# Kernel optimization log

Measured on AMD Instinct MI355X. Metric: run time of the kernel, lower is better.

The kernel has to match this reference:

```python
import jax, jax.numpy as jnp
import numpy as np

N_QUBITS = 10
T_STEPS = 10
NDATA = 1024
DIM = 2 ** N_QUBITS
PI = float(np.pi)


def setup_inputs() -> dict:
    key = jax.random.key(0)
    k1, k2, k3, k4, k5 = jax.random.split(key, 5)
    # random complex amplitudes (normalized to unit states inside reference)
    inputs_re = jax.random.normal(k1, (NDATA, DIM), dtype=jnp.float32)
    inputs_im = jax.random.normal(k2, (NDATA, DIM), dtype=jnp.float32)
    # diffusion noise schedule diff_hs (t,) in (0,1]
    diff_hs = jax.random.uniform(k5, (T_STEPS,), dtype=jnp.float32, minval=0.1, maxval=1.0)
    # var_1 = diff_hs.repeat(3n) in torch == tile -> index k scaled by diff_hs[k % t]
    var_1 = jnp.tile(diff_hs, 3 * N_QUBITS)                                  # (3*n*t,)
    phis = (jax.random.uniform(k3, (NDATA, 3 * N_QUBITS * T_STEPS), dtype=jnp.float32)
            * (PI / 4.0) - (PI / 8.0)) * var_1[None, :]
    gs = (jax.random.uniform(k4, (NDATA, T_STEPS), dtype=jnp.float32) * 0.2 + 0.4) * diff_hs[None, :]
    return {"inputs_re": inputs_re, "inputs_im": inputs_im, "phis": phis, "gs": gs}


def _apply_1q(psi, M, i):
    """Apply per-sample 2x2 gate M (B,2,2) on qubit i (qubit 0 = MSB) to psi (B, 2**n)."""
    left = 2 ** i
    right = 2 ** (N_QUBITS - 1 - i)
    s = psi.reshape(NDATA, left, 2, right)
    s = jnp.einsum('bxy,bayc->baxc', M, s)
    return s.reshape(NDATA, DIM)


def _scramble(inputs_re, inputs_im, phis, gs):
    n, t = N_QUBITS, T_STEPS
    psi = (inputs_re + 1j * inputs_im).astype(jnp.complex64)
    psi = psi / jnp.linalg.norm(psi, axis=1, keepdims=True)  # unit input states

    # precompute sum_{i<j} z_i z_j per basis state for the diagonal RZZ product
    idx = jnp.arange(DIM)
    bits = (idx[:, None] >> jnp.arange(n - 1, -1, -1)[None, :]) & 1  # (DIM, n), qubit0=MSB
    z = 1.0 - 2.0 * bits.astype(jnp.float32)
    zsum = z.sum(axis=1)
    pairsum = 0.5 * (zsum ** 2 - n)                                   # (DIM,)
    inv = 1.0 / (2.0 * np.sqrt(float(n)))

    for tt in range(t):
        base = 3 * n * tt
        for i in range(n):
            a = phis[:, base + i]            # first RZ angle
            th = phis[:, base + n + i]       # RY angle
            b = phis[:, base + 2 * n + i]    # second RZ angle
            c = jnp.cos(0.5 * th).astype(jnp.complex64)
            s = jnp.sin(0.5 * th).astype(jnp.complex64)
            ea_m = jnp.exp(-0.5j * a); ea_p = jnp.exp(0.5j * a)
            eb_m = jnp.exp(-0.5j * b); eb_p = jnp.exp(0.5j * b)
            # M = RZ(b) @ RY(th) @ RZ(a), per sample (B,2,2)
            M = jnp.stack([
                jnp.stack([eb_m * c * ea_m, -eb_m * s * ea_p], axis=-1),
                jnp.stack([eb_p * s * ea_m,  eb_p * c * ea_p], axis=-1),
            ], axis=-2)
            psi = _apply_1q(psi, M, i)
        # all RZZ(i,j, theta) gates are diagonal with shared theta -> single fused phase
        theta = (gs[:, tt] * inv).astype(jnp.complex64)
        psi = psi * jnp.exp(-0.5j * theta[:, None] * pairsum[None, :])
    return psi


def reference(inputs_re, inputs_im, phis, gs):
    psi = _scramble(inputs_re, inputs_im, phis, gs)
    return jnp.stack([psi.real, psi.imag])  # (2, Ndata, 2**n) float32
```

## Files before the change

### kernel.cpp

```cpp
#include <hip/hip_runtime.h>

#define NQ 10
#define TS 10
#define DIM 1024
#define ND 1024

typedef _Float16 h4 __attribute__((ext_vector_type(4)));
typedef __fp16  p2 __attribute__((ext_vector_type(2)));
typedef float f4 __attribute__((ext_vector_type(4)));

__device__ __forceinline__ f4 mfma16(h4 a, h4 b, f4 c) {
    return __builtin_amdgcn_mfma_f32_16x16x16f16(a, b, c, 0, 0, 0);
}
__device__ __forceinline__ h4 cvt_h4(f4 x) {
    p2 lo = __builtin_amdgcn_cvt_pkrtz(x[0], x[1]);
    p2 hi = __builtin_amdgcn_cvt_pkrtz(x[2], x[3]);
    h4 r; r[0] = lo[0]; r[1] = lo[1]; r[2] = hi[0]; r[3] = hi[1];
    return r;
}
__device__ __forceinline__ float xsgn(float v, unsigned m) {
    return __uint_as_float(__float_as_uint(v) ^ m);
}

__global__ __launch_bounds__(64, 1) void qsim_kernel(
    const float* __restrict__ re_in, const float* __restrict__ im_in,
    const float* __restrict__ phis, const float* __restrict__ gs,
    float* __restrict__ out)
{
    const int sample = blockIdx.x;
    const int lane = threadIdx.x;
    const int quad = lane >> 4;
    const int cc = lane & 15;
    const int c3 = (cc >> 3) & 1, c2 = (cc >> 2) & 1, c1 = (cc >> 1) & 1, c0 = cc & 1;
    const int q1 = quad >> 1, q0 = quad & 1;

    const bool e31 = (c3 == q1);
    const bool e20 = (c2 == q0);
    const bool bc1 = (c1 != 0);
    const bool bc0 = (c0 != 0);
    const unsigned sg3 = c3 ? 0u : 0x80000000u;
    const unsigned sg2 = c2 ? 0u : 0x80000000u;

    const float* pr_in = re_in + sample * DIM;
    const float* pi_in = im_in + sample * DIM;
    const float* ph = phis + sample * (3 * NQ * TS);
    const float* gsp = gs + sample * TS;

    f4 Sr[4], Si[4];
    const int lbase = 256 * quad + cc;
#pragma unroll
    for (int n = 0; n < 4; ++n)
#pragma unroll
        for (int s = 0; s < 4; ++s) {
            Sr[n][s] = pr_in[lbase + 64 * s + 16 * n];
            Si[n][s] = pi_in[lbase + 64 * s + 16 * n];
        }

    const float inv = 0.15811388300841897f;
    float gk[TS];
#pragma unroll
    for (int t = 0; t < TS; ++t) gk[t] = -0.5f * (gsp[t] * inv);

    float nrm = 0.f;
#pragma unroll
    for (int n = 0; n < 4; ++n)
#pragma unroll
        for (int s = 0; s < 4; ++s) nrm += Sr[n][s] * Sr[n][s] + Si[n][s] * Si[n][s];
#pragma unroll
    for (int off = 32; off >= 1; off >>= 1) nrm += __shfl_xor(nrm, off, 64);
    const float scl = rsqrtf(nrm);
#pragma unroll
    for (int n = 0; n < 4; ++n) { Sr[n] *= scl; Si[n] *= scl; }

    float psv[4][4];
    const int pbase = __popc(quad) + __popc(cc);
#pragma unroll
    for (int n = 0; n < 4; ++n)
#pragma unroll
        for (int s = 0; s < 4; ++s) {
            const int p = pbase + __popc(n) + __popc(s);
            const int z = NQ - 2 * p;
            psv[n][s] = 0.5f * (float)(z * z - NQ);
        }
    const float fq1 = (float)q1, fq0 = (float)q0;
    const float fc3 = (float)c3, fc2 = (float)c2, fc1 = (float)c1, fc0 = (float)c0;

    f4 DCPv[4], DSPv[4];
    h4 gbb[2];
    h4 hbb[2][4][4];
    float bcur[NQ];

    auto make_trig = [&](const float* v, float kcur) {
        float sv = 0.f;
#pragma unroll
        for (int i = 0; i < NQ; ++i) sv += v[i];
        float base = -0.5f * sv;
        base = fmaf(fq1, v[0], base); base = fmaf(fq0, v[1], base);
        base = fmaf(fc3, v[6], base); base = fmaf(fc2, v[7], base);
        base = fmaf(fc1, v[8], base); base = fmaf(fc0, v[9], base);
        const float addS[4] = {0.f, v[3], v[2], v[2] + v[3]};
        const float addN[4] = {0.f, v[5], v[4], v[4] + v[5]};
#pragma unroll
        for (int n = 0; n < 4; ++n)
#pragma unroll
            for (int s = 0; s < 4; ++s) {
                const float phi = fmaf(kcur, psv[n][s], base + addN[n] + addS[s]);
                float sp, cp;
                __sincosf(phi, &sp, &cp);
                DCPv[n][s] = cp;
                DSPv[n][s] = sp;
            }
    };

    auto make_tiles = [&](const float* th, h4& gbo, h4 (&hbo)[4][4]) {
        float C[NQ], S[NQ];
#pragma unroll
        for (int g = 0; g < NQ; ++g) {
            float sg, cg;
            __sincosf(0.5f * th[g], &sg, &cg);
            S[g] = sg; C[g] = cg;
        }
        {
            const float g0 = e31 ? C[0] : xsgn(S[0], sg3);
            const float g1 = e20 ? C[1] : xsgn(S[1], sg2);
            const float f01 = g0 * g1;
            const float A0 = bc1 ? S[2] : C[2];
            const float A1 = bc1 ? C[2] : -S[2];
            const float B0 = bc0 ? S[3] : C[3];
            const float B1 = bc0 ? C[3] : -S[3];
            p2 lo = __builtin_amdgcn_cvt_pkrtz(f01 * A0 * B0, f01 * A0 * B1);
            p2 hi = __builtin_amdgcn_cvt_pkrtz(f01 * A1 * B0, f01 * A1 * B1);
            gbo[0] = lo[0]; gbo[1] = lo[1]; gbo[2] = hi[0]; gbo[3] = hi[1];
        }
        const float F67 = (e31 ? C[6] : xsgn(S[6], sg3)) * (e20 ? C[7] : xsgn(S[7], sg2));
        const float A0p = bc1 ? S[8] : C[8];
        const float A1p = bc1 ? C[8] : -S[8];
        const float B0p = bc0 ? S[9] : C[9];
        const float B1p = bc0 ? C[9] : -S[9];
        float W[4];
        W[0] = F67 * A0p * B0p; W[1] = F67 * A0p * B1p;
        W[2] = F67 * A1p * B0p; W[3] = F67 * A1p * B1p;
        const float P4[4] = {C[4] * C[5], C[4] * S[5], S[4] * C[5], S[4] * S[5]};
        float TP[4][4];
#pragma unroll
        for (int k = 0; k < 4; ++k)
#pragma unroll
            for (int s = 0; s < 4; ++s) TP[k][s] = P4[k] * W[s];
#pragma unroll
        for (int n = 0; n < 4; ++n)
#pragma unroll
            for (int j = 0; j < 4; ++j) {
                const int n1 = n >> 1, n0 = n & 1, j1 = j >> 1, j0 = j & 1;
                const int d1 = n1 ^ j1, d0 = n0 ^ j0;
                const int idx = d1 * 2 + d0;
                const float sg = (((d1 && !n1) ? -1.f : 1.f) * ((d0 && !n0) ? -1.f : 1.f));
                p2 lo = __builtin_amdgcn_cvt_pkrtz(sg * TP[idx][0], sg * TP[idx][1]);
                p2 hi = __builtin_amdgcn_cvt_pkrtz(sg * TP[idx][2], sg * TP[idx][3]);
                hbo[n][j][0] = lo[0]; hbo[n][j][1] = lo[1];
                hbo[n][j][2] = hi[0]; hbo[n][j][3] = hi[1];
            }
    };

    {
        float phs0[30];
#pragma unroll
        for (int j = 0; j < 30; ++j) phs0[j] = ph[j];
        make_trig(&phs0[0], 0.f);
        make_tiles(&phs0[10], gbb[0], hbb[0]);
#pragma unroll
        for (int i = 0; i < NQ; ++i) bcur[i] = phs0[20 + i];
    }
    float pipe[2][30];
#pragma unroll
    for (int j = 0; j < 30; ++j) pipe[0][j] = ph[30 + j];

    const f4 zf4 = {0.f, 0.f, 0.f, 0.f};

#pragma unroll
    for (int tt = 0; tt < TS; ++tt) {
#pragma unroll
        for (int n = 0; n < 4; ++n) {
            const f4 xr = Sr[n], xi = Si[n];
            Sr[n] = DCPv[n] * xr - DSPv[n] * xi;
            Si[n] = DSPv[n] * xr + DCPv[n] * xi;
        }

        if (tt + 2 < TS) {
#pragma unroll
            for (int j = 0; j < 30; ++j) pipe[(tt + 1) & 1][j] = ph[30 * (tt + 2) + j];
        }

        h4 ar[4], ai[4];
#pragma unroll
        for (int n = 0; n < 4; ++n) { ar[n] = cvt_h4(Sr[n]); ai[n] = cvt_h4(Si[n]); }
        f4 Tr[4], Ti[4];
#pragma unroll
        for (int n = 0; n < 4; ++n) {
            Tr[n] = mfma16(ar[n], gbb[tt & 1], zf4);
            Ti[n] = mfma16(ai[n], gbb[tt & 1], zf4);
        }

        if (tt + 1 < TS) {
            const float* pN = pipe[tt & 1];
            float vN[NQ];
#pragma unroll
            for (int i = 0; i < NQ; ++i) vN[i] = pN[i] + bcur[i];
            make_trig(vN, gk[tt]);
            make_tiles(&pN[10], gbb[(tt + 1) & 1], hbb[(tt + 1) & 1]);
#pragma unroll
            for (int i = 0; i < NQ; ++i) bcur[i] = pN[20 + i];
        } else {
            make_trig(bcur, gk[TS - 1]);
        }

        h4 tr[4], ti[4];
#pragma unroll
        for (int n = 0; n < 4; ++n) { tr[n] = cvt_h4(Tr[n]); ti[n] = cvt_h4(Ti[n]); }
#pragma unroll
        for (int n = 0; n < 4; ++n) {
            f4 r0 = mfma16(tr[0], hbb[tt & 1][n][0], zf4);
            r0 = mfma16(tr[1], hbb[tt & 1][n][1], r0);
            f4 r1 = mfma16(tr[2], hbb[tt & 1][n][2], zf4);
            r1 = mfma16(tr[3], hbb[tt & 1][n][3], r1);
            f4 i0 = mfma16(ti[0], hbb[tt & 1][n][0], zf4);
            i0 = mfma16(ti[1], hbb[tt & 1][n][1], i0);
            f4 i1 = mfma16(ti[2], hbb[tt & 1][n][2], zf4);
            i1 = mfma16(ti[3], hbb[tt & 1][n][3], i1);
            Sr[n] = r0 + r1;
            Si[n] = i0 + i1;
        }
    }

#pragma unroll
    for (int n = 0; n < 4; ++n) {
        const f4 xr = Sr[n], xi = Si[n];
        Sr[n] = DCPv[n] * xr - DSPv[n] * xi;
        Si[n] = DSPv[n] * xr + DCPv[n] * xi;
    }

    float* outr = out + sample * DIM;
    float* outi = out + ND * DIM + sample * DIM;
#pragma unroll
    for (int n = 0; n < 4; ++n)
#pragma unroll
        for (int s = 0; s < 4; ++s) {
            outr[lbase + 64 * s + 16 * n] = Sr[n][s];
            outi[lbase + 64 * s + 16 * n] = Si[n][s];
        }
}

extern "C" void kernel_launch(void* const* d_in, const int* in_sizes, int n_in,
                              void* d_out, int out_size, void* d_ws, size_t ws_size,
                              hipStream_t stream) {
    const float* re_in = (const float*)d_in[0];
    const float* im_in = (const float*)d_in[1];
    const float* phis  = (const float*)d_in[2];
    const float* gs    = (const float*)d_in[3];
    float* out = (float*)d_out;
    qsim_kernel<<<ND, 64, 0, stream>>>(re_in, im_in, phis, gs, out);
}
```

Measured before the change: 77.47 us.

## Split each sample's state across two wavefronts with LDS exchange per step

Each block now runs two wavefronts that each hold half of the 1024 amplitudes. The norm is reduced across waves through shared memory, and after the first MFMA stage each wave writes its partial tiles to LDS so both can read all four tiles for the second stage. This halves per-wave register state and trig/tile work, which should raise occupancy and parallelism. The cost is one barrier and an LDS round trip per time step. The register double-buffered prefetch of phis is replaced by a plain load at the start of each step.

```diff
diff --git a/kernel.cpp b/kernel.cpp
--- a/kernel.cpp
+++ b/kernel.cpp
@@ -22,13 +22,15 @@
     return __uint_as_float(__float_as_uint(v) ^ m);
 }
 
-__global__ __launch_bounds__(64, 1) void qsim_kernel(
+__global__ __launch_bounds__(128, 2) void qsim_kernel(
     const float* __restrict__ re_in, const float* __restrict__ im_in,
     const float* __restrict__ phis, const float* __restrict__ gs,
     float* __restrict__ out)
 {
     const int sample = blockIdx.x;
-    const int lane = threadIdx.x;
+    const int tid  = threadIdx.x;
+    const int wid  = tid >> 6;
+    const int lane = tid & 63;
     const int quad = lane >> 4;
     const int cc = lane & 15;
     const int c3 = (cc >> 3) & 1, c2 = (cc >> 2) & 1, c1 = (cc >> 1) & 1, c0 = cc & 1;
@@ -41,19 +43,23 @@
     const unsigned sg3 = c3 ? 0u : 0x80000000u;
     const unsigned sg2 = c2 ? 0u : 0x80000000u;
 
+    __shared__ h4 xch[2][4][2][64];
+    __shared__ float nsh[2];
+
     const float* pr_in = re_in + sample * DIM;
     const float* pi_in = im_in + sample * DIM;
     const float* ph = phis + sample * (3 * NQ * TS);
     const float* gsp = gs + sample * TS;
 
-    f4 Sr[4], Si[4];
+    f4 Sr[2], Si[2];
     const int lbase = 256 * quad + cc;
-#pragma unroll
-    for (int n = 0; n < 4; ++n)
+    const int noff = 32 * wid;
+#pragma unroll
+    for (int m = 0; m < 2; ++m)
 #pragma unroll
         for (int s = 0; s < 4; ++s) {
-            Sr[n][s] = pr_in[lbase + 64 * s + 16 * n];
-            Si[n][s] = pi_in[lbase + 64 * s + 16 * n];
+            Sr[m][s] = pr_in[lbase + 64 * s + noff + 16 * m];
+            Si[m][s] = pi_in[lbase + 64 * s + noff + 16 * m];
         }
 
     const float inv = 0.15811388300841897f;
@@ -63,31 +69,34 @@
 
     float nrm = 0.f;
 #pragma unroll
-    for (int n = 0; n < 4; ++n)
-#pragma unroll
-        for (int s = 0; s < 4; ++s) nrm += Sr[n][s] * Sr[n][s] + Si[n][s] * Si[n][s];
+    for (int m = 0; m < 2; ++m)
+#pragma unroll
+        for (int s = 0; s < 4; ++s) nrm += Sr[m][s] * Sr[m][s] + Si[m][s] * Si[m][s];
 #pragma unroll
     for (int off = 32; off >= 1; off >>= 1) nrm += __shfl_xor(nrm, off, 64);
-    const float scl = rsqrtf(nrm);
-#pragma unroll
-    for (int n = 0; n < 4; ++n) { Sr[n] *= scl; Si[n] *= scl; }
-
-    float psv[4][4];
-    const int pbase = __popc(quad) + __popc(cc);
-#pragma unroll
-    for (int n = 0; n < 4; ++n)
+    if (lane == 0) nsh[wid] = nrm;
+    __syncthreads();
+    const float scl = rsqrtf(nsh[0] + nsh[1]);
+#pragma unroll
+    for (int m = 0; m < 2; ++m) { Sr[m] *= scl; Si[m] *= scl; }
+
+    float psv[2][4];
+    const int pbase = __popc(quad) + __popc(cc) + wid;
+#pragma unroll
+    for (int m = 0; m < 2; ++m)
 #pragma unroll
         for (int s = 0; s < 4; ++s) {
-            const int p = pbase + __popc(n) + __popc(s);
+            const int p = pbase + m + __popc(s);
             const int z = NQ - 2 * p;
-            psv[n][s] = 0.5f * (float)(z * z - NQ);
+            psv[m][s] = 0.5f * (float)(z * z - NQ);
         }
     const float fq1 = (float)q1, fq0 = (float)q0;
     const float fc3 = (float)c3, fc2 = (float)c2, fc1 = (float)c1, fc0 = (float)c0;
-
-    f4 DCPv[4], DSPv[4];
+    const float fwid = (float)wid;
+
+    f4 DCPv[2], DSPv[2];
     h4 gbb[2];
-    h4 hbb[2][4][4];
+    h4 hbb[2][2][4];
     float bcur[NQ];
 
     auto make_trig = [&](const float* v, float kcur) {
@@ -98,21 +107,23 @@
         base = fmaf(fq1, v[0], base); base = fmaf(fq0, v[1], base);
         base = fmaf(fc3, v[6], base); base = fmaf(fc2, v[7], base);
         base = fmaf(fc1, v[8], base); base = fmaf(fc0, v[9], base);
+        base = fmaf(fwid, v[4], base);
         const float addS[4] = {0.f, v[3], v[2], v[2] + v[3]};
-        const float addN[4] = {0.f, v[5], v[4], v[4] + v[5]};
-#pragma unroll
-        for (int n = 0; n < 4; ++n)
+#pragma unroll
+        for (int m = 0; m < 2; ++m) {
+            const float bm = base + (m ? v[5] : 0.f);
 #pragma unroll
             for (int s = 0; s < 4; ++s) {
-                const float phi = fmaf(kcur, psv[n][s], base + addN[n] + addS[s]);
+                const float phi = fmaf(kcur, psv[m][s], bm + addS[s]);
                 float sp, cp;
                 __sincosf(phi, &sp, &cp);
-                DCPv[n][s] = cp;
-                DSPv[n][s] = sp;
+                DCPv[m][s] = cp;
+                DSPv[m][s] = sp;
             }
+        }
     };
 
-    auto make_tiles = [&](const float* th, h4& gbo, h4 (&hbo)[4][4]) {
+    auto make_tiles = [&](const float* th, h4& gbo, h4 (&hbo)[2][4]) {
         float C[NQ], S[NQ];
 #pragma unroll
         for (int g = 0; g < NQ; ++g) {
@@ -140,25 +151,21 @@
         float W[4];
         W[0] = F67 * A0p * B0p; W[1] = F67 * A0p * B1p;
         W[2] = F67 * A1p * B0p; W[3] = F67 * A1p * B1p;
-        const float P4[4] = {C[4] * C[5], C[4] * S[5], S[4] * C[5], S[4] * S[5]};
-        float TP[4][4];
-#pragma unroll
-        for (int k = 0; k < 4; ++k)
-#pragma unroll
-            for (int s = 0; s < 4; ++s) TP[k][s] = P4[k] * W[s];
-#pragma unroll
-        for (int n = 0; n < 4; ++n)
+        const float s4_0 = wid ? S[4] : C[4];
+        const float s4_1 = wid ? C[4] : -S[4];
+#pragma unroll
+        for (int m = 0; m < 2; ++m) {
+            const float s5_0 = m ? S[5] : C[5];
+            const float s5_1 = m ? C[5] : -S[5];
 #pragma unroll
             for (int j = 0; j < 4; ++j) {
-                const int n1 = n >> 1, n0 = n & 1, j1 = j >> 1, j0 = j & 1;
-                const int d1 = n1 ^ j1, d0 = n0 ^ j0;
-                const int idx = d1 * 2 + d0;
-                const float sg = (((d1 && !n1) ? -1.f : 1.f) * ((d0 && !n0) ? -1.f : 1.f));
-                p2 lo = __builtin_amdgcn_cvt_pkrtz(sg * TP[idx][0], sg * TP[idx][1]);
-                p2 hi = __builtin_amdgcn_cvt_pkrtz(sg * TP[idx][2], sg * TP[idx][3]);
-                hbo[n][j][0] = lo[0]; hbo[n][j][1] = lo[1];
-                hbo[n][j][2] = hi[0]; hbo[n][j][3] = hi[1];
+                const float v45 = ((j >> 1) ? s4_1 : s4_0) * ((j & 1) ? s5_1 : s5_0);
+                p2 lo = __builtin_amdgcn_cvt_pkrtz(v45 * W[0], v45 * W[1]);
+                p2 hi = __builtin_amdgcn_cvt_pkrtz(v45 * W[2], v45 * W[3]);
+                hbo[m][j][0] = lo[0]; hbo[m][j][1] = lo[1];
+                hbo[m][j][2] = hi[0]; hbo[m][j][3] = hi[1];
             }
+        }
     };
 
     {
@@ -170,82 +177,91 @@
 #pragma unroll
         for (int i = 0; i < NQ; ++i) bcur[i] = phs0[20 + i];
     }
-    float pipe[2][30];
-#pragma unroll
-    for (int j = 0; j < 30; ++j) pipe[0][j] = ph[30 + j];
 
     const f4 zf4 = {0.f, 0.f, 0.f, 0.f};
 
 #pragma unroll
     for (int tt = 0; tt < TS; ++tt) {
-#pragma unroll
-        for (int n = 0; n < 4; ++n) {
-            const f4 xr = Sr[n], xi = Si[n];
-            Sr[n] = DCPv[n] * xr - DSPv[n] * xi;
-            Si[n] = DSPv[n] * xr + DCPv[n] * xi;
-        }
-
-        if (tt + 2 < TS) {
-#pragma unroll
-            for (int j = 0; j < 30; ++j) pipe[(tt + 1) & 1][j] = ph[30 * (tt + 2) + j];
-        }
-
-        h4 ar[4], ai[4];
-#pragma unroll
-        for (int n = 0; n < 4; ++n) { ar[n] = cvt_h4(Sr[n]); ai[n] = cvt_h4(Si[n]); }
-        f4 Tr[4], Ti[4];
-#pragma unroll
-        for (int n = 0; n < 4; ++n) {
-            Tr[n] = mfma16(ar[n], gbb[tt & 1], zf4);
-            Ti[n] = mfma16(ai[n], gbb[tt & 1], zf4);
-        }
-
+        const int cb = tt & 1, nb = cb ^ 1;
+
+        float pn[30];
         if (tt + 1 < TS) {
-            const float* pN = pipe[tt & 1];
+#pragma unroll
+            for (int j = 0; j < 30; ++j) pn[j] = ph[30 * (tt + 1) + j];
+        }
+
+#pragma unroll
+        for (int m = 0; m < 2; ++m) {
+            const f4 xr = Sr[m], xi = Si[m];
+            Sr[m] = DCPv[m] * xr - DSPv[m] * xi;
+            Si[m] = DSPv[m] * xr + DCPv[m] * xi;
+        }
+
+        h4 tr[2], ti[2];
+#pragma unroll
+        for (int m = 0; m < 2; ++m) {
+            f4 Trm = mfma16(cvt_h4(Sr[m]), gbb[cb], zf4);
+            f4 Tim = mfma16(cvt_h4(Si[m]), gbb[cb], zf4);
+            tr[m] = cvt_h4(Trm);
+            ti[m] = cvt_h4(Tim);
+        }
+
+#pragma unroll
+        for (int m = 0; m < 2; ++m) {
+            xch[cb][2 * wid + m][0][lane] = tr[m];
+            xch[cb][2 * wid + m][1][lane] = ti[m];
+        }
+        __syncthreads();
+
+        h4 trA[4], tiA[4];
+#pragma unroll
+        for (int j = 0; j < 4; ++j) {
+            trA[j] = xch[cb][j][0][lane];
+            tiA[j] = xch[cb][j][1][lane];
+        }
+
+        if (tt + 1 < TS) {
             float vN[NQ];
 #pragma unroll
-            for (int i = 0; i < NQ; ++i) vN[i] = pN[i] + bcur[i];
+            for (int i = 0; i < NQ; ++i) vN[i] = pn[i] + bcur[i];
             make_trig(vN, gk[tt]);
-            make_tiles(&pN[10], gbb[(tt + 1) & 1], hbb[(tt + 1) & 1]);
-#pragma unroll
-            for (int i = 0; i < NQ; ++i) bcur[i] = pN[20 + i];
+            make_tiles(&pn[10], gbb[nb], hbb[nb]);
+#pragma unroll
+            for (int i = 0; i < NQ; ++i) bcur[i] = pn[20 + i];
         } else {
             make_trig(bcur, gk[TS - 1]);
         }
 
-        h4 tr[4], ti[4];
-#pragma unroll
-        for (int n = 0; n < 4; ++n) { tr[n] = cvt_h4(Tr[n]); ti[n] = cvt_h4(Ti[n]); }
-#pragma unroll
-        for (int n = 0; n < 4; ++n) {
-            f4 r0 = mfma16(tr[0], hbb[tt & 1][n][0], zf4);
-            r0 = mfma16(tr[1], hbb[tt & 1][n][1], r0);
-            f4 r1 = mfma16(tr[2], hbb[tt & 1][n][2], zf4);
-            r1 = mfma16(tr[3], hbb[tt & 1][n][3], r1);
-            f4 i0 = mfma16(ti[0], hbb[tt & 1][n][0], zf4);
-            i0 = mfma16(ti[1], hbb[tt & 1][n][1], i0);
-            f4 i1 = mfma16(ti[2], hbb[tt & 1][n][2], zf4);
-            i1 = mfma16(ti[3], hbb[tt & 1][n][3], i1);
-            Sr[n] = r0 + r1;
-            Si[n] = i0 + i1;
+#pragma unroll
+        for (int m = 0; m < 2; ++m) {
+            f4 r0 = mfma16(trA[0], hbb[cb][m][0], zf4);
+            r0 = mfma16(trA[1], hbb[cb][m][1], r0);
+            f4 r1 = mfma16(trA[2], hbb[cb][m][2], zf4);
+            r1 = mfma16(trA[3], hbb[cb][m][3], r1);
+            f4 i0 = mfma16(tiA[0], hbb[cb][m][0], zf4);
+            i0 = mfma16(tiA[1], hbb[cb][m][1], i0);
+            f4 i1 = mfma16(tiA[2], hbb[cb][m][2], zf4);
+            i1 = mfma16(tiA[3], hbb[cb][m][3], i1);
+            Sr[m] = r0 + r1;
+            Si[m] = i0 + i1;
         }
     }
 
 #pragma unroll
-    for (int n = 0; n < 4; ++n) {
-        const f4 xr = Sr[n], xi = Si[n];
-        Sr[n] = DCPv[n] * xr - DSPv[n] * xi;
-        Si[n] = DSPv[n] * xr + DCPv[n] * xi;
+    for (int m = 0; m < 2; ++m) {
+        const f4 xr = Sr[m], xi = Si[m];
+        Sr[m] = DCPv[m] * xr - DSPv[m] * xi;
+        Si[m] = DSPv[m] * xr + DCPv[m] * xi;
     }
 
     float* outr = out + sample * DIM;
     float* outi = out + ND * DIM + sample * DIM;
 #pragma unroll
-    for (int n = 0; n < 4; ++n)
+    for (int m = 0; m < 2; ++m)
 #pragma unroll
         for (int s = 0; s < 4; ++s) {
-            outr[lbase + 64 * s + 16 * n] = Sr[n][s];
-            outi[lbase + 64 * s + 16 * n] = Si[n][s];
+            outr[lbase + 64 * s + noff + 16 * m] = Sr[m][s];
+            outi[lbase + 64 * s + noff + 16 * m] = Si[m][s];
         }
 }
 
@@ -257,5 +273,5 @@
     const float* phis  = (const float*)d_in[2];
     const float* gs    = (const float*)d_in[3];
     float* out = (float*)d_out;
-    qsim_kernel<<<ND, 64, 0, stream>>>(re_in, im_in, phis, gs, out);
-}
+    qsim_kernel<<<ND, 128, 0, stream>>>(re_in, im_in, phis, gs, out);
+}
```

After: 79.16 us. 2.2% more time.
